# Kernel tuning notes

Hardware: AMD Instinct MI355X
Metric: run time of the kernel (lower is better)

The kernel has to match this reference:

```python
import jax, jax.numpy as jnp
import numpy as np

EMB_DIM = 1024
ATTN_DIM = 1024


def setup_inputs() -> dict:
    key = jax.random.key(0)
    k_x, k_wk, k_wq, k_wv = jax.random.split(key, 4)
    bound = 1.0 / np.sqrt(EMB_DIM)  # nn.Linear default init range
    return {
        "embedded": jax.random.normal(k_x, (4, 2048, EMB_DIM), dtype=jnp.float32),
        "W_k": jax.random.uniform(k_wk, (ATTN_DIM, EMB_DIM), jnp.float32, -bound, bound),
        "W_q": jax.random.uniform(k_wq, (ATTN_DIM, EMB_DIM), jnp.float32, -bound, bound),
        "W_v": jax.random.uniform(k_wv, (ATTN_DIM, EMB_DIM), jnp.float32, -bound, bound),
    }


def reference(embedded, W_k, W_q, W_v):
    # Linear (bias=False): y = x @ W.T
    K = jnp.einsum("bse,ae->bsa", embedded, W_k)
    Q = jnp.einsum("bse,ae->bsa", embedded, W_q)
    V = jnp.einsum("bse,ae->bsa", embedded, W_v)
    S = K.shape[1]
    scale = 1.0 / jnp.sqrt(jnp.float32(ATTN_DIM))
    scores = jnp.einsum("bqa,bka->bqk", Q, K) * scale  # [B, S, S]
    causal = jnp.tril(jnp.ones((S, S), dtype=bool))  # True = keep
    scores = jnp.where(causal[None, :, :], scores, -jnp.inf)
    attn = jax.nn.softmax(scores, axis=2)
    out = jnp.einsum("bqk,bka->bqa", attn, V)
    # torch.round(x, decimals=4)
    return jnp.round(out * 1e4) / 1e4
```

## Files before the change

### kernel.cpp

```cpp
#include <hip/hip_runtime.h>
#include <stdint.h>

#define B_ 4
#define S_ 2048
#define E_ 1024
#define D_ 1024

typedef short  bf16x8 __attribute__((ext_vector_type(8)));
typedef float  f32x4  __attribute__((ext_vector_type(4)));

static __device__ __forceinline__ unsigned short f2bf(float f) {
    unsigned int u = __float_as_uint(f);
    u += 0x7fffu + ((u >> 16) & 1u);
    return (unsigned short)(u >> 16);
}

static __device__ __forceinline__ void async16(const unsigned short* g, unsigned short* l) {
    auto gp = (const __attribute__((address_space(1))) void*)(uintptr_t)g;
    auto lp = (__attribute__((address_space(3))) void*)(uintptr_t)l;
    __builtin_amdgcn_global_load_lds(gp, lp, 16, 0, 0);
}


__global__ __launch_bounds__(256)
void convert_kernel(const float* __restrict__ x,  const float* __restrict__ Wk,
                    const float* __restrict__ Wq, const float* __restrict__ Wv,
                    unsigned short* __restrict__ xb, unsigned short* __restrict__ Wb)
{
    const long long idx = ((long long)blockIdx.x * 256 + threadIdx.x) * 4;
    const float* src; unsigned short* dst; long long off;
    if (idx < (long long)B_ * S_ * E_) {
        src = x; dst = xb; off = idx;
    } else {
        long long w = idx - (long long)B_ * S_ * E_;
        const int sel = (int)(w >> 20);
        off = w & 1048575LL;
        src = (sel == 0) ? Wk : (sel == 1) ? Wq : Wv;
        dst = Wb + ((long long)sel << 20);
    }
    const float4 f = *(const float4*)(src + off);
    ushort4 u = { f2bf(f.x), f2bf(f.y), f2bf(f.z), f2bf(f.w) };
    *(ushort4*)(dst + off) = u;
}

__global__ __launch_bounds__(256, 4)
void proj_kernel(const unsigned short* __restrict__ xb,
                 const unsigned short* __restrict__ Wb,
                 unsigned short* __restrict__ Qb,
                 unsigned short* __restrict__ Kb,
                 unsigned short* __restrict__ Vt)
{
    __shared__ __align__(16) unsigned short As[128 * 64];
    __shared__ __align__(16) unsigned short Bs[128 * 64];

    const int t    = threadIdx.x;
    const int m0   = blockIdx.x * 128;
    const int ny   = blockIdx.y;
    const int wsel = ny >> 3;
    const int nloc = (ny & 7) * 128;

    const int lane = t & 63, wave = t >> 6;
    const int l15 = lane & 15, quad = lane >> 4;
    const int wm = wave & 1, wn = wave >> 1;
    const int sr = lane >> 3;
    const int sq = ((lane & 7) ^ sr) * 8;
    const int l7 = l15 & 7;
    const int rcA0 = (wm * 64 + l15) * 64 + ((quad ^ l7) * 8);
    const int rcA1 = (wm * 64 + l15) * 64 + (((4 + quad) ^ l7) * 8);
    const int rcB0 = (wn * 64 + l15) * 64 + ((quad ^ l7) * 8);
    const int rcB1 = (wn * 64 + l15) * 64 + (((4 + quad) ^ l7) * 8);

    const unsigned short* gA = xb + (size_t)(m0 + wave * 32 + sr) * E_ + sq;
    const unsigned short* gB = Wb + (size_t)(ny * 128 + wave * 32 + sr) * E_ + sq;
    unsigned short* lA = &As[wave * 2048];
    unsigned short* lB = &Bs[wave * 2048];

    f32x4 acc[4][4];
    #pragma unroll
    for (int i = 0; i < 4; i++)
        #pragma unroll
        for (int j = 0; j < 4; j++) acc[i][j] = {0.f, 0.f, 0.f, 0.f};

    for (int k0 = 0; k0 < E_; k0 += 64) {
        __syncthreads();
        #pragma unroll
        for (int i = 0; i < 4; i++) {
            async16(gA + k0 + i * 8 * E_, lA + i * 512);
            async16(gB + k0 + i * 8 * E_, lB + i * 512);
        }
        __syncthreads();

        #pragma unroll
        for (int s = 0; s < 2; s++) {
            bf16x8 af[4], bfr[4];
            const int ra = s ? rcA1 : rcA0, rb = s ? rcB1 : rcB0;
            #pragma unroll
            for (int i = 0; i < 4; i++) af[i]  = *(const bf16x8*)&As[ra + i * 1024];
            #pragma unroll
            for (int j = 0; j < 4; j++) bfr[j] = *(const bf16x8*)&Bs[rb + j * 1024];
            #pragma unroll
            for (int i = 0; i < 4; i++)
                #pragma unroll
                for (int j = 0; j < 4; j++)
                    acc[i][j] = __builtin_amdgcn_mfma_f32_16x16x32_bf16(af[i], bfr[j], acc[i][j], 0, 0, 0);
        }
    }

    if (wsel == 0) {
        #pragma unroll
        for (int i = 0; i < 4; i++)
            #pragma unroll
            for (int j = 0; j < 4; j++) {
                const int gn = nloc + wn * 64 + j * 16 + l15;
                #pragma unroll
                for (int r = 0; r < 4; r++) {
                    const int gm = m0 + wm * 64 + i * 16 + quad * 4 + r;
                    Kb[(size_t)gm * D_ + gn] = f2bf(acc[i][j][r]);
                }
            }
    } else if (wsel == 1) {
        #pragma unroll
        for (int i = 0; i < 4; i++)
            #pragma unroll
            for (int j = 0; j < 4; j++) {
                const int gn = nloc + wn * 64 + j * 16 + l15;
                #pragma unroll
                for (int r = 0; r < 4; r++) {
                    const int gm = m0 + wm * 64 + i * 16 + quad * 4 + r;
                    Qb[(size_t)gm * D_ + gn] = f2bf(acc[i][j][r] * 0.03125f);
                }
            }
    } else {
        #pragma unroll
        for (int i = 0; i < 4; i++)
            #pragma unroll
            for (int j = 0; j < 4; j++) {
                const int s0 = m0 + wm * 64 + i * 16 + quad * 4;
                const int b  = s0 >> 11, sl = s0 & (S_ - 1);
                const int gn = nloc + wn * 64 + j * 16 + l15;
                ushort4 u = { f2bf(acc[i][j][0]), f2bf(acc[i][j][1]),
                              f2bf(acc[i][j][2]), f2bf(acc[i][j][3]) };
                *(ushort4*)&Vt[((size_t)(b << 10) + gn) * S_ + sl] = u;
            }
    }
}

__global__ __launch_bounds__(256, 2)
void expscores_kernel(const unsigned short* __restrict__ Qb,
                      const unsigned short* __restrict__ Kb,
                      unsigned short* __restrict__ P,
                      float* __restrict__ rowpart)
{
    const int nt = blockIdx.x;
    const int mt = 15 - blockIdx.y;
    const int b  = blockIdx.z;
    if (nt > mt) return;

    __shared__ __align__(16) unsigned short As[2 * 128 * 64];
    __shared__ __align__(16) unsigned short Bs[2 * 128 * 64];

    const int t = threadIdx.x;
    const int m0 = mt * 128, n0 = nt * 128;

    const int lane = t & 63, wave = t >> 6;
    const int l15 = lane & 15, quad = lane >> 4;
    const int wm = wave & 1, wn = wave >> 1;
    const int sr = lane >> 3;
    const int sq = ((lane & 7) ^ sr) * 8;
    const int l7 = l15 & 7;

    const unsigned short* gA = Qb + (size_t)b * S_ * D_ + (size_t)(m0 + wave * 32 + sr) * D_ + sq;
    const unsigned short* gB = Kb + (size_t)b * S_ * D_ + (size_t)(n0 + wave * 32 + sr) * D_ + sq;
    unsigned short* lA = &As[wave * 2048];
    unsigned short* lB = &Bs[wave * 2048];

    f32x4 acc[4][4];
    #pragma unroll
    for (int i = 0; i < 4; i++)
        #pragma unroll
        for (int j = 0; j < 4; j++) acc[i][j] = {0.f, 0.f, 0.f, 0.f};

    #pragma unroll
    for (int i = 0; i < 4; i++) {
        async16(gA + i * 8 * D_, lA + i * 512);
        async16(gB + i * 8 * D_, lB + i * 512);
    }

    int buf = 0;
    for (int kt = 0; kt < 16; kt++) {
        __syncthreads();
        if (kt < 15) {
            const int k0 = (kt + 1) * 64;
            const int nb = (buf ^ 1) * 8192;
            #pragma unroll
            for (int i = 0; i < 4; i++) {
                async16(gA + k0 + i * 8 * D_, lA + nb + i * 512);
                async16(gB + k0 + i * 8 * D_, lB + nb + i * 512);
            }
        }
        const unsigned short* Ac = As + buf * 8192;
        const unsigned short* Bc = Bs + buf * 8192;
        #pragma unroll
        for (int s = 0; s < 2; s++) {
            const int cs = ((s * 4 + quad) ^ l7) * 8;
            bf16x8 af[4], bfr[4];
            #pragma unroll
            for (int i = 0; i < 4; i++)
                af[i] = *(const bf16x8*)&Ac[(wm * 64 + i * 16 + l15) * 64 + cs];
            #pragma unroll
            for (int j = 0; j < 4; j++)
                bfr[j] = *(const bf16x8*)&Bc[(wn * 64 + j * 16 + l15) * 64 + cs];
            #pragma unroll
            for (int i = 0; i < 4; i++)
                #pragma unroll
                for (int j = 0; j < 4; j++)
                    acc[i][j] = __builtin_amdgcn_mfma_f32_16x16x32_bf16(af[i], bfr[j], acc[i][j], 0, 0, 0);
        }
        buf ^= 1;
    }

    unsigned short* Pb = P + (size_t)b * S_ * S_;
    #pragma unroll
    for (int i = 0; i < 4; i++)
        #pragma unroll
        for (int j = 0; j < 4; j++) {
            const int gn = n0 + wn * 64 + j * 16 + l15;
            #pragma unroll
            for (int r = 0; r < 4; r++) {
                const int gm = m0 + wm * 64 + i * 16 + quad * 4 + r;
                const float e = (gn <= gm) ? __expf(acc[i][j][r]) : 0.f;
                acc[i][j][r] = e;
                Pb[(size_t)gm * S_ + gn] = f2bf(e);
            }
        }

    float* rp = rowpart + ((size_t)b * 32 + nt * 2 + wn) * S_;
    #pragma unroll
    for (int i = 0; i < 4; i++) {
        float rsub[4];
        #pragma unroll
        for (int r = 0; r < 4; r++) {
            float s = acc[i][0][r] + acc[i][1][r] + acc[i][2][r] + acc[i][3][r];
            #pragma unroll
            for (int off = 8; off; off >>= 1) s += __shfl_xor(s, off);
            rsub[r] = s;
        }
        if (l15 == 0) {
            #pragma unroll
            for (int r = 0; r < 4; r++)
                rp[m0 + wm * 64 + i * 16 + quad * 4 + r] = rsub[r];
        }
    }
}

__global__ __launch_bounds__(256, 2)
void pv_kernel(const unsigned short* __restrict__ P,
               const unsigned short* __restrict__ Vt,
               const float* __restrict__ rowpart,
               float* __restrict__ out)
{
    const int nt = blockIdx.x;
    const int mt = 15 - blockIdx.y;
    const int b  = blockIdx.z;

    __shared__ __align__(16) unsigned short As[2 * 128 * 64];
    __shared__ __align__(16) unsigned short Bs[2 * 128 * 64];

    const int t = threadIdx.x;
    const int m0 = mt * 128, n0 = nt * 128;
    const int niter = 2 * mt + 2;

    const int lane = t & 63, wave = t >> 6;
    const int l15 = lane & 15, quad = lane >> 4;
    const int wm = wave & 1, wn = wave >> 1;
    const int sr = lane >> 3;
    const int sq = ((lane & 7) ^ sr) * 8;
    const int l7 = l15 & 7;

    const unsigned short* gA = P  + (size_t)b * S_ * S_ + (size_t)(m0 + wave * 32 + sr) * S_ + sq;
    const unsigned short* gB = Vt + (size_t)b * D_ * S_ + (size_t)(n0 + wave * 32 + sr) * S_ + sq;
    unsigned short* lA = &As[wave * 2048];
    unsigned short* lB = &Bs[wave * 2048];

    f32x4 acc[4][4];
    #pragma unroll
    for (int i = 0; i < 4; i++)
        #pragma unroll
        for (int j = 0; j < 4; j++) acc[i][j] = {0.f, 0.f, 0.f, 0.f};

    #pragma unroll
    for (int i = 0; i < 4; i++) {
        async16(gA + i * 8 * S_, lA + i * 512);
        async16(gB + i * 8 * S_, lB + i * 512);
    }

    int buf = 0;
    for (int kt = 0; kt < niter; kt++) {
        __syncthreads();
        if (kt + 1 < niter) {
            const int k0 = (kt + 1) * 64;
            const int nb = (buf ^ 1) * 8192;
            #pragma unroll
            for (int i = 0; i < 4; i++) {
                async16(gA + k0 + i * 8 * S_, lA + nb + i * 512);
                async16(gB + k0 + i * 8 * S_, lB + nb + i * 512);
            }
        }
        const unsigned short* Ac = As + buf * 8192;
        const unsigned short* Bc = Bs + buf * 8192;
        #pragma unroll
        for (int s = 0; s < 2; s++) {
            const int cs = ((s * 4 + quad) ^ l7) * 8;
            bf16x8 af[4], bfr[4];
            #pragma unroll
            for (int i = 0; i < 4; i++)
                af[i] = *(const bf16x8*)&Ac[(wm * 64 + i * 16 + l15) * 64 + cs];
            #pragma unroll
            for (int j = 0; j < 4; j++)
                bfr[j] = *(const bf16x8*)&Bc[(wn * 64 + j * 16 + l15) * 64 + cs];
            #pragma unroll
            for (int i = 0; i < 4; i++)
                #pragma unroll
                for (int j = 0; j < 4; j++)
                    acc[i][j] = __builtin_amdgcn_mfma_f32_16x16x32_bf16(af[i], bfr[j], acc[i][j], 0, 0, 0);
        }
        buf ^= 1;
    }

    const int nsl = 2 * mt + 2;
    const float* rp = rowpart + (size_t)b * 32 * S_ + (m0 + wm * 64 + lane);
    float rsum = 0.f;
    for (int k = 0; k < nsl; k++) rsum += rp[(size_t)k * S_];
    const float invr = 1.0f / rsum;

    #pragma unroll
    for (int i = 0; i < 4; i++) {
        #pragma unroll
        for (int r = 0; r < 4; r++) {
            const float vr = __shfl(invr, i * 16 + quad * 4 + r);
            const int gm = m0 + wm * 64 + i * 16 + quad * 4 + r;
            #pragma unroll
            for (int j = 0; j < 4; j++) {
                const int gn = n0 + wn * 64 + j * 16 + l15;
                out[((size_t)b * S_ + gm) * D_ + gn] = rintf(acc[i][j][r] * vr * 1e4f) * 1e-4f;
            }
        }
    }
}

extern "C" void kernel_launch(void* const* d_in, const int* in_sizes, int n_in,
                              void* d_out, int out_size, void* d_ws, size_t ws_size,
                              hipStream_t stream)
{
    (void)in_sizes; (void)n_in; (void)out_size; (void)ws_size;
    const float* x  = (const float*)d_in[0];
    const float* Wk = (const float*)d_in[1];
    const float* Wq = (const float*)d_in[2];
    const float* Wv = (const float*)d_in[3];
    float* out = (float*)d_out;

    char* ws = (char*)d_ws;
    unsigned short* Qb = (unsigned short*)ws;
    unsigned short* Kb = Qb + (size_t)B_ * S_ * D_;
    unsigned short* Vt = Kb + (size_t)B_ * S_ * D_;
    unsigned short* P  = Vt + (size_t)B_ * D_ * S_;
    unsigned short* xb = P;
    unsigned short* Wb = xb + (size_t)B_ * S_ * E_;
    float* rowpart = (float*)(P + (size_t)B_ * S_ * S_);

    const int conv_blocks = (B_ * S_ * E_ + 3 * D_ * E_) / (256 * 4);
    convert_kernel  <<<conv_blocks, 256, 0, stream>>>(x, Wk, Wq, Wv, xb, Wb);
    proj_kernel     <<<dim3(64, 24, 1),   256, 0, stream>>>(xb, Wb, Qb, Kb, Vt);
    expscores_kernel<<<dim3(16, 16, B_),  256, 0, stream>>>(Qb, Kb, P, rowpart);
    pv_kernel       <<<dim3(8, 16, B_),   256, 0, stream>>>(P, Vt, rowpart, out);
}
```

Baseline: 223.9 us.

## Single-buffer expscores LDS for higher occupancy and alternate pv tile order per batch

Result: faster. 216.1 us (-3.5%).

```diff
diff --git a/kernel.cpp b/kernel.cpp
--- a/kernel.cpp
+++ b/kernel.cpp
@@ -145,7 +145,7 @@
     }
 }
 
-__global__ __launch_bounds__(256, 2)
+__global__ __launch_bounds__(256, 4)
 void expscores_kernel(const unsigned short* __restrict__ Qb,
                       const unsigned short* __restrict__ Kb,
                       unsigned short* __restrict__ P,
@@ -156,8 +156,8 @@
     const int b  = blockIdx.z;
     if (nt > mt) return;
 
-    __shared__ __align__(16) unsigned short As[2 * 128 * 64];
-    __shared__ __align__(16) unsigned short Bs[2 * 128 * 64];
+    __shared__ __align__(16) unsigned short As[128 * 64];
+    __shared__ __align__(16) unsigned short Bs[128 * 64];
 
     const int t = threadIdx.x;
     const int m0 = mt * 128, n0 = nt * 128;
@@ -180,43 +180,32 @@
         #pragma unroll
         for (int j = 0; j < 4; j++) acc[i][j] = {0.f, 0.f, 0.f, 0.f};
 
-    #pragma unroll
-    for (int i = 0; i < 4; i++) {
-        async16(gA + i * 8 * D_, lA + i * 512);
-        async16(gB + i * 8 * D_, lB + i * 512);
-    }
-
-    int buf = 0;
     for (int kt = 0; kt < 16; kt++) {
-        __syncthreads();
-        if (kt < 15) {
-            const int k0 = (kt + 1) * 64;
-            const int nb = (buf ^ 1) * 8192;
-            #pragma unroll
-            for (int i = 0; i < 4; i++) {
-                async16(gA + k0 + i * 8 * D_, lA + nb + i * 512);
-                async16(gB + k0 + i * 8 * D_, lB + nb + i * 512);
-            }
-        }
-        const unsigned short* Ac = As + buf * 8192;
-        const unsigned short* Bc = Bs + buf * 8192;
+        const int k0 = kt * 64;
+        __syncthreads();
+        #pragma unroll
+        for (int i = 0; i < 4; i++) {
+            async16(gA + k0 + i * 8 * D_, lA + i * 512);
+            async16(gB + k0 + i * 8 * D_, lB + i * 512);
+        }
+        __syncthreads();
+
         #pragma unroll
         for (int s = 0; s < 2; s++) {
             const int cs = ((s * 4 + quad) ^ l7) * 8;
             bf16x8 af[4], bfr[4];
             #pragma unroll
             for (int i = 0; i < 4; i++)
-                af[i] = *(const bf16x8*)&Ac[(wm * 64 + i * 16 + l15) * 64 + cs];
+                af[i] = *(const bf16x8*)&As[(wm * 64 + i * 16 + l15) * 64 + cs];
             #pragma unroll
             for (int j = 0; j < 4; j++)
-                bfr[j] = *(const bf16x8*)&Bc[(wn * 64 + j * 16 + l15) * 64 + cs];
+                bfr[j] = *(const bf16x8*)&Bs[(wn * 64 + j * 16 + l15) * 64 + cs];
             #pragma unroll
             for (int i = 0; i < 4; i++)
                 #pragma unroll
                 for (int j = 0; j < 4; j++)
                     acc[i][j] = __builtin_amdgcn_mfma_f32_16x16x32_bf16(af[i], bfr[j], acc[i][j], 0, 0, 0);
         }
-        buf ^= 1;
     }
 
     unsigned short* Pb = P + (size_t)b * S_ * S_;
@@ -260,8 +249,9 @@
                float* __restrict__ out)
 {
     const int nt = blockIdx.x;
-    const int mt = 15 - blockIdx.y;
+    const int yy = blockIdx.y;
     const int b  = blockIdx.z;
+    const int mt = (b & 2) ? yy : (15 - yy);
 
     __shared__ __align__(16) unsigned short As[2 * 128 * 64];
     __shared__ __align__(16) unsigned short Bs[2 * 128 * 64];
```
